# Optimization experiments

Hardware: AMD Instinct MI355X
Metric: run time of the kernel (lower is better)

Reference implementation:

```python
import jax, jax.numpy as jnp
import numpy as np

WS = 7      # window size (square)
HD = 32     # head_dim
NH = 12     # n_heads = input_dim // head_dim = 384 // 32
C = 384     # input_dim == output_dim


def _rel_bias(rel_pos):
    # rel_pos: (NH, 2*WS-1, 2*WS-1) -> bias (NH, WS*WS, WS*WS)
    coords = np.stack(np.meshgrid(np.arange(WS), np.arange(WS), indexing='ij'), -1).reshape(-1, 2)
    rel = coords[:, None, :] - coords[None, :, :]  # (49, 49, 2)
    return rel_pos[:, rel[..., 0] + WS - 1, rel[..., 1] + WS - 1]


def setup_inputs() -> dict:
    key = jax.random.key(0)
    ks = jax.random.split(key, 5)
    x = jax.random.normal(ks[0], (32, 56, 56, C), jnp.float32)
    w_qkv = jax.random.normal(ks[1], (C, 3 * C), jnp.float32) * 0.02
    b_qkv = jnp.zeros((3 * C,), jnp.float32)
    rel_pos = jax.random.normal(ks[2], (NH, 2 * WS - 1, 2 * WS - 1), jnp.float32) * 0.02
    w_out = jax.random.normal(ks[3], (C, C), jnp.float32) * 0.02
    b_out = jnp.zeros((C,), jnp.float32)
    return {"x": x, "w_qkv": w_qkv, "b_qkv": b_qkv, "rel_pos": rel_pos,
            "w_out": w_out, "b_out": b_out}


def reference(x, w_qkv, b_qkv, rel_pos, w_out, b_out):
    b, H, W, c = x.shape
    hw, ww = H // WS, W // WS
    nw, p = hw * ww, WS * WS
    # window partition: b (w1 p1) (w2 p2) c -> b (w1 w2) (p1 p2) c
    xw = x.reshape(b, hw, WS, ww, WS, c).transpose(0, 1, 3, 2, 4, 5).reshape(b, nw, p, c)
    # fused QKV projection; layout (3, NH, HD) along last dim matches torch chunk over threeh
    qkv = (xw @ w_qkv + b_qkv).reshape(b, nw, p, 3, NH, HD)
    q, k, v = qkv[..., 0, :, :], qkv[..., 1, :, :], qkv[..., 2, :, :]
    scale = HD ** -0.5
    sim = jnp.einsum('bwphc,bwqhc->bwhpq', q, k) * scale  # (b, nw, NH, p, p)
    sim = sim + _rel_bias(rel_pos)[None, None]
    probs = jax.nn.softmax(sim, axis=-1)
    out = jnp.einsum('bwhpq,bwqhc->bwphc', probs, v).reshape(b, nw, p, NH * HD)
    out = out @ w_out + b_out
    # window merge: b (w1 w2) (p1 p2) c -> b (w1 p1) (w2 p2) c
    out = out.reshape(b, hw, ww, WS, WS, -1).transpose(0, 1, 3, 2, 4, 5).reshape(b, H, W, -1)
    return out
```

## Files before the change

kernel.cpp:

```cpp
#include <hip/hip_runtime.h>
#include <cstdint>

typedef __bf16 bf16_t;
typedef __bf16 bf16x8 __attribute__((ext_vector_type(8)));
typedef __bf16 bf16x4 __attribute__((ext_vector_type(4)));
typedef float  f32x4  __attribute__((ext_vector_type(4)));

#define DEV static __device__ __forceinline__

DEV void load_lds16(const void* g, void* l) {
  __builtin_amdgcn_global_load_lds(
      (__attribute__((address_space(1))) void*)(uintptr_t)g,
      (__attribute__((address_space(3))) void*)l, 16, 0, 0);
}

__global__ __launch_bounds__(256) void cvt_x_kernel(const float* __restrict__ x,
                                                    bf16_t* __restrict__ xb, int n4) {
  int i = blockIdx.x * 256 + threadIdx.x;
  const int stride = gridDim.x * 256;
  for (; i < n4; i += stride) {
    float4 v = ((const float4*)x)[i];
    bf16x4 o;
    o[0] = (bf16_t)v.x; o[1] = (bf16_t)v.y; o[2] = (bf16_t)v.z; o[3] = (bf16_t)v.w;
    ((bf16x4*)xb)[i] = o;
  }
}

__global__ __launch_bounds__(256) void prep_small_kernel(const float* __restrict__ wqkv,
                                                         const float* __restrict__ wout,
                                                         const float* __restrict__ rel_pos,
                                                         bf16_t* __restrict__ wqkvT,
                                                         bf16_t* __restrict__ woutT,
                                                         float* __restrict__ bias) {
  int i = blockIdx.x * 256 + threadIdx.x;
  if (i < 1152 * 384) {
    int n = i / 384, k = i % 384;
    wqkvT[i] = (bf16_t)wqkv[k * 1152 + n];
    return;
  }
  i -= 1152 * 384;
  if (i < 384 * 384) {
    int n = i / 384, k = i % 384;
    woutT[i] = (bf16_t)wout[k * 384 + n];
    return;
  }
  i -= 384 * 384;
  if (i < 12 * 49 * 49) {
    int h = i / 2401, r = i % 2401;
    int p = r / 49, q = r % 49;
    int py = p / 7, px = p % 7, qy = q / 7, qx = q % 7;
    bias[i] = rel_pos[h * 169 + (py - qy + 6) * 13 + (px - qx + 6)];
  }
}

template <int N, int K, bool OUT_BF16>
__global__ __launch_bounds__(256) void gemm_kernel(const bf16_t* __restrict__ A,
                                                   const bf16_t* __restrict__ BT,
                                                   const float* __restrict__ bias,
                                                   void* __restrict__ Cout) {
  constexpr int BK = 64;
  __shared__ bf16_t sA[128][BK];
  __shared__ bf16_t sB[128][BK];
  constexpr int NT = N / 128;
  const int mt = blockIdx.x / NT, nt = blockIdx.x % NT;
  const int m0 = mt * 128, n0 = nt * 128;
  const int tid = threadIdx.x;
  const int lane = tid & 63;
  const int wid = tid >> 6;
  const int wr = (wid >> 1) * 64, wc = (wid & 1) * 64;
  const int lr = lane & 15, lg = lane >> 4;
  f32x4 acc[4][4] = {};
  for (int k0 = 0; k0 < K; k0 += BK) {
    #pragma unroll
    for (int i = 0; i < 4; ++i) {
      const int linear = i * 256 + tid;
      const int row = linear >> 3, un = linear & 7;
      load_lds16(A  + (size_t)(m0 + row) * K + k0 + un * 8, ((bf16_t*)sA) + (size_t)linear * 8);
      load_lds16(BT + (size_t)(n0 + row) * K + k0 + un * 8, ((bf16_t*)sB) + (size_t)linear * 8);
    }
    __syncthreads();
    #pragma unroll
    for (int k2 = 0; k2 < BK; k2 += 32) {
      bf16x8 af[4], bfr[4];
      #pragma unroll
      for (int mi = 0; mi < 4; ++mi)
        af[mi] = *(const bf16x8*)&sA[wr + mi * 16 + lr][k2 + lg * 8];
      #pragma unroll
      for (int ni = 0; ni < 4; ++ni)
        bfr[ni] = *(const bf16x8*)&sB[wc + ni * 16 + lr][k2 + lg * 8];
      #pragma unroll
      for (int mi = 0; mi < 4; ++mi)
        #pragma unroll
        for (int ni = 0; ni < 4; ++ni)
          acc[mi][ni] = __builtin_amdgcn_mfma_f32_16x16x32_bf16(af[mi], bfr[ni], acc[mi][ni], 0, 0, 0);
    }
    __syncthreads();
  }
  #pragma unroll
  for (int ni = 0; ni < 4; ++ni) {
    const int c = n0 + wc + ni * 16 + lr;
    const float bv = bias[c];
    #pragma unroll
    for (int mi = 0; mi < 4; ++mi) {
      const int r0 = m0 + wr + mi * 16 + lg * 4;
      #pragma unroll
      for (int rg = 0; rg < 4; ++rg) {
        const float v = acc[mi][ni][rg] + bv;
        if constexpr (OUT_BF16)
          ((bf16_t*)Cout)[(size_t)(r0 + rg) * N + c] = (bf16_t)v;
        else
          ((float*)Cout)[(size_t)(r0 + rg) * N + c] = v;
      }
    }
  }
}

__global__ __launch_bounds__(256) void attn_kernel(const bf16_t* __restrict__ qkv,
                                                   const float* __restrict__ bias,
                                                   bf16_t* __restrict__ aout) {
  __shared__ bf16_t P_lds[4][64][64];
  const int tid = threadIdx.x, lane = tid & 63, w = tid >> 6;
  const int pair = blockIdx.x * 4 + w;
  const int win = pair / 12, h = pair % 12;
  const int b = win >> 6, wy = (win >> 3) & 7, wx = win & 7;
  const int tbase = b * 3136 + wy * 392 + wx * 7;
  const int lr = lane & 15, lg = lane >> 4;
  const float scale = 0.17677669529663687f;

  bf16x8 qf[4], kf[4];
  #pragma unroll
  for (int mi = 0; mi < 4; ++mi) {
    const int p = mi * 16 + lr;
    bf16x8 z = {};
    if (p < 49) {
      const int t = tbase + (p / 7) * 56 + (p % 7);
      const size_t base = (size_t)t * 1152 + h * 32 + lg * 8;
      qf[mi] = *(const bf16x8*)(qkv + base);
      kf[mi] = *(const bf16x8*)(qkv + base + 384);
    } else { qf[mi] = z; kf[mi] = z; }
  }

  f32x4 s[4][4] = {};
  #pragma unroll
  for (int mi = 0; mi < 4; ++mi)
    #pragma unroll
    for (int ni = 0; ni < 4; ++ni)
      s[mi][ni] = __builtin_amdgcn_mfma_f32_16x16x32_bf16(qf[mi], kf[ni], s[mi][ni], 0, 0, 0);

  #pragma unroll
  for (int mi = 0; mi < 4; ++mi) {
    #pragma unroll
    for (int rg = 0; rg < 4; ++rg) {
      const int rr = mi * 16 + lg * 4 + rg;
      const float* brow = bias + (size_t)h * 2401 + rr * 49;
      float vv[4];
      #pragma unroll
      for (int ni = 0; ni < 4; ++ni) {
        const int c = ni * 16 + lr;
        float v = s[mi][ni][rg] * scale;
        if (c < 49) { if (rr < 49) v += brow[c]; }
        else v = -1e30f;
        vv[ni] = v;
      }
      float m = fmaxf(fmaxf(vv[0], vv[1]), fmaxf(vv[2], vv[3]));
      #pragma unroll
      for (int off = 1; off < 16; off <<= 1) m = fmaxf(m, __shfl_xor(m, off, 64));
      float sum = 0.f;
      #pragma unroll
      for (int ni = 0; ni < 4; ++ni) { const float e = __expf(vv[ni] - m); vv[ni] = e; sum += e; }
      #pragma unroll
      for (int off = 1; off < 16; off <<= 1) sum += __shfl_xor(sum, off, 64);
      const float inv = 1.f / sum;
      #pragma unroll
      for (int ni = 0; ni < 4; ++ni) s[mi][ni][rg] = vv[ni] * inv;
    }
  }

  #pragma unroll
  for (int mi = 0; mi < 4; ++mi)
    #pragma unroll
    for (int ni = 0; ni < 4; ++ni)
      #pragma unroll
      for (int rg = 0; rg < 4; ++rg)
        P_lds[w][mi * 16 + lg * 4 + rg][ni * 16 + lr] = (bf16_t)s[mi][ni][rg];
  asm volatile("s_waitcnt lgkmcnt(0)" ::: "memory");

  f32x4 o[4][2] = {};
  #pragma unroll
  for (int s2 = 0; s2 < 2; ++s2) {
    bf16x8 vfr[2];
    #pragma unroll
    for (int ni = 0; ni < 2; ++ni) {
      #pragma unroll
      for (int j = 0; j < 8; ++j) {
        const int kq = s2 * 32 + lg * 8 + j;
        if (kq < 49) {
          const int t = tbase + (kq / 7) * 56 + (kq % 7);
          vfr[ni][j] = qkv[(size_t)t * 1152 + 768 + h * 32 + ni * 16 + lr];
        } else vfr[ni][j] = (bf16_t)0.f;
      }
    }
    bf16x8 pf[4];
    #pragma unroll
    for (int mi = 0; mi < 4; ++mi)
      pf[mi] = *(const bf16x8*)&P_lds[w][mi * 16 + lr][s2 * 32 + lg * 8];
    #pragma unroll
    for (int mi = 0; mi < 4; ++mi)
      #pragma unroll
      for (int ni = 0; ni < 2; ++ni)
        o[mi][ni] = __builtin_amdgcn_mfma_f32_16x16x32_bf16(pf[mi], vfr[ni], o[mi][ni], 0, 0, 0);
  }

  #pragma unroll
  for (int mi = 0; mi < 4; ++mi)
    #pragma unroll
    for (int rg = 0; rg < 4; ++rg) {
      const int p = mi * 16 + lg * 4 + rg;
      if (p < 49) {
        const int t = tbase + (p / 7) * 56 + (p % 7);
        #pragma unroll
        for (int ni = 0; ni < 2; ++ni)
          aout[(size_t)t * 384 + h * 32 + ni * 16 + lr] = (bf16_t)o[mi][ni][rg];
      }
    }
}

extern "C" void kernel_launch(void* const* d_in, const int* in_sizes, int n_in,
                              void* d_out, int out_size, void* d_ws, size_t ws_size,
                              hipStream_t stream) {
  const float* x       = (const float*)d_in[0];
  const float* w_qkv   = (const float*)d_in[1];
  const float* b_qkv   = (const float*)d_in[2];
  const float* rel_pos = (const float*)d_in[3];
  const float* w_out   = (const float*)d_in[4];
  const float* b_out   = (const float*)d_in[5];
  float* out = (float*)d_out;

  char* ws = (char*)d_ws;
  const size_t QKV_B = 231211008ull;
  const size_t XB_B  = 77070336ull;
  bf16_t* qkv   = (bf16_t*)ws;
  bf16_t* xb    = (bf16_t*)(ws + QKV_B);
  bf16_t* wqkvT = (bf16_t*)(ws + QKV_B + XB_B);
  bf16_t* woutT = (bf16_t*)(ws + QKV_B + XB_B + 884736);
  float*  bias  = (float*)(ws + QKV_B + XB_B + 884736 + 294912);

  cvt_x_kernel<<<2048, 256, 0, stream>>>(x, xb, 38535168 / 4);
  prep_small_kernel<<<(1152 * 384 + 384 * 384 + 12 * 49 * 49 + 255) / 256, 256, 0, stream>>>(
      w_qkv, w_out, rel_pos, wqkvT, woutT, bias);
  gemm_kernel<1152, 384, true><<<784 * 9, 256, 0, stream>>>(xb, wqkvT, b_qkv, qkv);
  attn_kernel<<<6144, 256, 0, stream>>>(qkv, bias, xb);
  gemm_kernel<384, 384, false><<<784 * 3, 256, 0, stream>>>(xb, woutT, b_out, out);
}
```

Baseline: 668.7 us.

## Store QKV in window-major per-head layout and stage GEMM epilogues through LDS

The QKV GEMM now scatters its output through LDS into a window/head-contiguous layout (each head's q, k and v block for a window is 49x32 contiguous). The attention kernel can then read q/k with simple contiguous loads and bulk-load V into LDS instead of doing scalar strided gathers. Both GEMMs stage their epilogue through shared memory so global stores are 16-byte vectors, and blocks are swizzled by groups of 8. The cost is extra LDS traffic and syncs in the epilogues, and padded rows now read clamped duplicates instead of zeros, which relies on the padded P columns being zero.

```diff
diff --git a/kernel.cpp b/kernel.cpp
--- a/kernel.cpp
+++ b/kernel.cpp
@@ -53,20 +53,105 @@
   }
 }
 
-template <int N, int K, bool OUT_BF16>
-__global__ __launch_bounds__(256) void gemm_kernel(const bf16_t* __restrict__ A,
-                                                   const bf16_t* __restrict__ BT,
-                                                   const float* __restrict__ bias,
-                                                   void* __restrict__ Cout) {
-  constexpr int BK = 64;
-  __shared__ bf16_t sA[128][BK];
-  __shared__ bf16_t sB[128][BK];
-  constexpr int NT = N / 128;
-  const int mt = blockIdx.x / NT, nt = blockIdx.x % NT;
+#define WIN_STRIDE 56448
+#define HP_STRIDE  1568
+
+__global__ __launch_bounds__(256) void gemm_qkv_kernel(const bf16_t* __restrict__ A,
+                                                       const bf16_t* __restrict__ BT,
+                                                       const float* __restrict__ bias,
+                                                       bf16_t* __restrict__ qkvw) {
+  constexpr int NT = 9, K = 384, BK = 64;
+  __shared__ __align__(16) bf16_t smem[16384];
+  __shared__ int rowmap[128];
+  bf16_t* sA = smem;
+  bf16_t* sB = smem + 8192;
+  int bid = blockIdx.x;
+  bid = (bid & 7) * 882 + (bid >> 3);
+  const int mt = bid / NT, nt = bid % NT;
   const int m0 = mt * 128, n0 = nt * 128;
   const int tid = threadIdx.x;
-  const int lane = tid & 63;
-  const int wid = tid >> 6;
+  const int lane = tid & 63, wid = tid >> 6;
+  const int wr = (wid >> 1) * 64, wc = (wid & 1) * 64;
+  const int lr = lane & 15, lg = lane >> 4;
+
+  if (tid < 128) {
+    const int t = m0 + tid;
+    const int b = t / 3136, r2 = t - b * 3136;
+    const int y = r2 / 56, x = r2 - y * 56;
+    const int win = b * 64 + (y / 7) * 8 + (x / 7);
+    const int q = (y % 7) * 7 + (x % 7);
+    rowmap[tid] = win * WIN_STRIDE + q * 32;
+  }
+
+  f32x4 acc[4][4] = {};
+  for (int k0 = 0; k0 < K; k0 += BK) {
+    #pragma unroll
+    for (int i = 0; i < 4; ++i) {
+      const int linear = i * 256 + tid;
+      const int row = linear >> 3, un = linear & 7;
+      load_lds16(A  + (size_t)(m0 + row) * K + k0 + un * 8, sA + linear * 8);
+      load_lds16(BT + (size_t)(n0 + row) * K + k0 + un * 8, sB + linear * 8);
+    }
+    __syncthreads();
+    #pragma unroll
+    for (int k2 = 0; k2 < BK; k2 += 32) {
+      bf16x8 af[4], bfr[4];
+      #pragma unroll
+      for (int mi = 0; mi < 4; ++mi)
+        af[mi] = *(const bf16x8*)&sA[(wr + mi * 16 + lr) * BK + k2 + lg * 8];
+      #pragma unroll
+      for (int ni = 0; ni < 4; ++ni)
+        bfr[ni] = *(const bf16x8*)&sB[(wc + ni * 16 + lr) * BK + k2 + lg * 8];
+      #pragma unroll
+      for (int mi = 0; mi < 4; ++mi)
+        #pragma unroll
+        for (int ni = 0; ni < 4; ++ni)
+          acc[mi][ni] = __builtin_amdgcn_mfma_f32_16x16x32_bf16(af[mi], bfr[ni], acc[mi][ni], 0, 0, 0);
+    }
+    __syncthreads();
+  }
+  bf16_t* sC = smem;
+  #pragma unroll
+  for (int ni = 0; ni < 4; ++ni) {
+    const int cl = wc + ni * 16 + lr;
+    const float bv = bias[n0 + cl];
+    #pragma unroll
+    for (int mi = 0; mi < 4; ++mi) {
+      const int r0 = wr + mi * 16 + lg * 4;
+      #pragma unroll
+      for (int rg = 0; rg < 4; ++rg)
+        sC[(r0 + rg) * 128 + cl] = (bf16_t)(acc[mi][ni][rg] + bv);
+    }
+  }
+  __syncthreads();
+  #pragma unroll
+  for (int it = 0; it < 8; ++it) {
+    const int linear = it * 256 + tid;
+    const int row = linear >> 4, u = linear & 15;
+    bf16x8 val = *(const bf16x8*)&sC[row * 128 + u * 8];
+    const int c0 = n0 + u * 8;
+    const int part = c0 >= 768 ? 2 : (c0 >= 384 ? 1 : 0);
+    const int cp = c0 - part * 384;
+    const int h = cp >> 5, d0 = cp & 31;
+    *(bf16x8*)(qkvw + (size_t)rowmap[row] + (h * 3 + part) * HP_STRIDE + d0) = val;
+  }
+}
+
+__global__ __launch_bounds__(256) void gemm_out_kernel(const bf16_t* __restrict__ A,
+                                                       const bf16_t* __restrict__ BT,
+                                                       const float* __restrict__ bias,
+                                                       float* __restrict__ Cout) {
+  constexpr int NT = 3, N = 384, K = 384, BK = 64;
+  __shared__ __align__(16) bf16_t smem[16384];
+  bf16_t* sA = smem;
+  bf16_t* sB = smem + 8192;
+  float* sCf = (float*)smem;
+  int bid = blockIdx.x;
+  bid = (bid & 7) * 294 + (bid >> 3);
+  const int mt = bid / NT, nt = bid % NT;
+  const int m0 = mt * 128, n0 = nt * 128;
+  const int tid = threadIdx.x;
+  const int lane = tid & 63, wid = tid >> 6;
   const int wr = (wid >> 1) * 64, wc = (wid & 1) * 64;
   const int lr = lane & 15, lg = lane >> 4;
   f32x4 acc[4][4] = {};
@@ -75,8 +160,8 @@
     for (int i = 0; i < 4; ++i) {
       const int linear = i * 256 + tid;
       const int row = linear >> 3, un = linear & 7;
-      load_lds16(A  + (size_t)(m0 + row) * K + k0 + un * 8, ((bf16_t*)sA) + (size_t)linear * 8);
-      load_lds16(BT + (size_t)(n0 + row) * K + k0 + un * 8, ((bf16_t*)sB) + (size_t)linear * 8);
+      load_lds16(A  + (size_t)(m0 + row) * K + k0 + un * 8, sA + linear * 8);
+      load_lds16(BT + (size_t)(n0 + row) * K + k0 + un * 8, sB + linear * 8);
     }
     __syncthreads();
     #pragma unroll
@@ -84,10 +169,10 @@
       bf16x8 af[4], bfr[4];
       #pragma unroll
       for (int mi = 0; mi < 4; ++mi)
-        af[mi] = *(const bf16x8*)&sA[wr + mi * 16 + lr][k2 + lg * 8];
+        af[mi] = *(const bf16x8*)&sA[(wr + mi * 16 + lr) * BK + k2 + lg * 8];
       #pragma unroll
       for (int ni = 0; ni < 4; ++ni)
-        bfr[ni] = *(const bf16x8*)&sB[wc + ni * 16 + lr][k2 + lg * 8];
+        bfr[ni] = *(const bf16x8*)&sB[(wc + ni * 16 + lr) * BK + k2 + lg * 8];
       #pragma unroll
       for (int mi = 0; mi < 4; ++mi)
         #pragma unroll
@@ -97,28 +182,38 @@
     __syncthreads();
   }
   #pragma unroll
-  for (int ni = 0; ni < 4; ++ni) {
-    const int c = n0 + wc + ni * 16 + lr;
-    const float bv = bias[c];
-    #pragma unroll
-    for (int mi = 0; mi < 4; ++mi) {
-      const int r0 = m0 + wr + mi * 16 + lg * 4;
-      #pragma unroll
-      for (int rg = 0; rg < 4; ++rg) {
-        const float v = acc[mi][ni][rg] + bv;
-        if constexpr (OUT_BF16)
-          ((bf16_t*)Cout)[(size_t)(r0 + rg) * N + c] = (bf16_t)v;
-        else
-          ((float*)Cout)[(size_t)(r0 + rg) * N + c] = v;
+  for (int hp = 0; hp < 2; ++hp) {
+    if ((wid >> 1) == hp) {
+      #pragma unroll
+      for (int ni = 0; ni < 4; ++ni) {
+        const int cl = wc + ni * 16 + lr;
+        const float bv = bias[n0 + cl];
+        #pragma unroll
+        for (int mi = 0; mi < 4; ++mi) {
+          const int r0 = mi * 16 + lg * 4;
+          #pragma unroll
+          for (int rg = 0; rg < 4; ++rg)
+            sCf[(r0 + rg) * 128 + cl] = acc[mi][ni][rg] + bv;
+        }
       }
     }
-  }
-}
-
-__global__ __launch_bounds__(256) void attn_kernel(const bf16_t* __restrict__ qkv,
+    __syncthreads();
+    #pragma unroll
+    for (int it = 0; it < 8; ++it) {
+      const int linear = it * 256 + tid;
+      const int row = linear >> 5, u = linear & 31;
+      f32x4 v = *(const f32x4*)&sCf[row * 128 + u * 4];
+      *(f32x4*)(Cout + (size_t)(m0 + hp * 64 + row) * 384 + n0 + u * 4) = v;
+    }
+    __syncthreads();
+  }
+}
+
+__global__ __launch_bounds__(256) void attn_kernel(const bf16_t* __restrict__ qkvw,
                                                    const float* __restrict__ bias,
                                                    bf16_t* __restrict__ aout) {
-  __shared__ bf16_t P_lds[4][64][64];
+  __shared__ __align__(16) bf16_t P_lds[4][64][64];
+  __shared__ __align__(16) bf16_t v_lds[4][64][32];
   const int tid = threadIdx.x, lane = tid & 63, w = tid >> 6;
   const int pair = blockIdx.x * 4 + w;
   const int win = pair / 12, h = pair % 12;
@@ -126,18 +221,23 @@
   const int tbase = b * 3136 + wy * 392 + wx * 7;
   const int lr = lane & 15, lg = lane >> 4;
   const float scale = 0.17677669529663687f;
+  const bf16_t* base = qkvw + (size_t)win * WIN_STRIDE + (size_t)h * 3 * HP_STRIDE;
+
+  {
+    const bf16_t* vsrc = base + 2 * HP_STRIDE;
+    bf16_t* vdst = &v_lds[w][0][0];
+    #pragma unroll
+    for (int c = 0; c < 4; ++c)
+      load_lds16(vsrc + c * 512 + lane * 8, vdst + c * 512 + lane * 8);
+  }
 
   bf16x8 qf[4], kf[4];
   #pragma unroll
   for (int mi = 0; mi < 4; ++mi) {
     const int p = mi * 16 + lr;
-    bf16x8 z = {};
-    if (p < 49) {
-      const int t = tbase + (p / 7) * 56 + (p % 7);
-      const size_t base = (size_t)t * 1152 + h * 32 + lg * 8;
-      qf[mi] = *(const bf16x8*)(qkv + base);
-      kf[mi] = *(const bf16x8*)(qkv + base + 384);
-    } else { qf[mi] = z; kf[mi] = z; }
+    const int pq = p < 49 ? p : 48;
+    qf[mi] = *(const bf16x8*)(base + pq * 32 + lg * 8);
+    kf[mi] = *(const bf16x8*)(base + HP_STRIDE + pq * 32 + lg * 8);
   }
 
   f32x4 s[4][4] = {};
@@ -183,23 +283,19 @@
       #pragma unroll
       for (int rg = 0; rg < 4; ++rg)
         P_lds[w][mi * 16 + lg * 4 + rg][ni * 16 + lr] = (bf16_t)s[mi][ni][rg];
-  asm volatile("s_waitcnt lgkmcnt(0)" ::: "memory");
+
+  asm volatile("s_waitcnt vmcnt(0) lgkmcnt(0)" ::: "memory");
+  __builtin_amdgcn_sched_barrier(0);
 
   f32x4 o[4][2] = {};
   #pragma unroll
   for (int s2 = 0; s2 < 2; ++s2) {
     bf16x8 vfr[2];
     #pragma unroll
-    for (int ni = 0; ni < 2; ++ni) {
-      #pragma unroll
-      for (int j = 0; j < 8; ++j) {
-        const int kq = s2 * 32 + lg * 8 + j;
-        if (kq < 49) {
-          const int t = tbase + (kq / 7) * 56 + (kq % 7);
-          vfr[ni][j] = qkv[(size_t)t * 1152 + 768 + h * 32 + ni * 16 + lr];
-        } else vfr[ni][j] = (bf16_t)0.f;
-      }
-    }
+    for (int ni = 0; ni < 2; ++ni)
+      #pragma unroll
+      for (int j = 0; j < 8; ++j)
+        vfr[ni][j] = v_lds[w][s2 * 32 + lg * 8 + j][ni * 16 + lr];
     bf16x8 pf[4];
     #pragma unroll
     for (int mi = 0; mi < 4; ++mi)
@@ -237,18 +333,18 @@
   float* out = (float*)d_out;
 
   char* ws = (char*)d_ws;
-  const size_t QKV_B = 231211008ull;
-  const size_t XB_B  = 77070336ull;
-  bf16_t* qkv   = (bf16_t*)ws;
-  bf16_t* xb    = (bf16_t*)(ws + QKV_B);
-  bf16_t* wqkvT = (bf16_t*)(ws + QKV_B + XB_B);
-  bf16_t* woutT = (bf16_t*)(ws + QKV_B + XB_B + 884736);
-  float*  bias  = (float*)(ws + QKV_B + XB_B + 884736 + 294912);
+  const size_t QKVW_B = 231211008ull;
+  const size_t XB_B   = 77070336ull;
+  bf16_t* qkvw  = (bf16_t*)ws;
+  bf16_t* xb    = (bf16_t*)(ws + QKVW_B);
+  bf16_t* wqkvT = (bf16_t*)(ws + QKVW_B + XB_B);
+  bf16_t* woutT = (bf16_t*)(ws + QKVW_B + XB_B + 884736);
+  float*  bias  = (float*)(ws + QKVW_B + XB_B + 884736 + 294912);
 
   cvt_x_kernel<<<2048, 256, 0, stream>>>(x, xb, 38535168 / 4);
   prep_small_kernel<<<(1152 * 384 + 384 * 384 + 12 * 49 * 49 + 255) / 256, 256, 0, stream>>>(
       w_qkv, w_out, rel_pos, wqkvT, woutT, bias);
-  gemm_kernel<1152, 384, true><<<784 * 9, 256, 0, stream>>>(xb, wqkvT, b_qkv, qkv);
-  attn_kernel<<<6144, 256, 0, stream>>>(qkv, bias, xb);
-  gemm_kernel<384, 384, false><<<784 * 3, 256, 0, stream>>>(xb, woutT, b_out, out);
-}
+  gemm_qkv_kernel<<<784 * 9, 256, 0, stream>>>(xb, wqkvT, b_qkv, qkvw);
+  attn_kernel<<<6144, 256, 0, stream>>>(qkvw, bias, xb);
+  gemm_out_kernel<<<784 * 3, 256, 0, stream>>>(xb, woutT, b_out, out);
+}
```

After: 661.2 us. About the same (-1.1%).
